# Kernel tuning notes

Measured on AMD Instinct MI355X. Metric: run time of the kernel, lower is better.

Reference implementation:

```python
import jax, jax.numpy as jnp
import numpy as np

BANDS = 103
FEATURE_DIM = 20
NSPIX = 256
N_ITER = 5
EPS = 1e-8


def _conv(x, w):
    # NCHW conv, SAME padding, stride 1
    return jax.lax.conv_general_dilated(x, w, (1, 1), 'SAME',
                                         dimension_numbers=('NCHW', 'OIHW', 'NCHW'))


def _aconv_bn_relu(x, k7, k5, k3, b, g, beta):
    # AConv: parallel 7x7 + 5x5 + 3x3 convs summed, then BatchNorm (batch stats) + ReLU
    y = _conv(x, k7) + _conv(x, k5) + _conv(x, k3) + b[None, :, None, None]
    mu = y.mean(axis=(0, 2, 3), keepdims=True)
    var = y.var(axis=(0, 2, 3), keepdims=True)
    y = (y - mu) * jax.lax.rsqrt(var + 1e-5) * g[None, :, None, None] + beta[None, :, None, None]
    return jax.nn.relu(y)


def _lsg_iter(pf, nspix, n_iter):
    # SSN-style iterative superpixel clustering.
    # pf: [B, C, H, W] pixel features. Returns soft assignment Q: [B, nspix, H*W].
    B, C, H, W = pf.shape
    hs = ws = int(np.sqrt(nspix))
    # init centroids by block-averaging onto an hs x ws grid
    c0 = pf.reshape(B, C, hs, H // hs, ws, W // ws).mean(axis=(3, 5)).reshape(B, C, nspix)
    pix = pf.reshape(B, C, H * W)            # [B, C, N]
    pn2 = jnp.sum(pix * pix, axis=1)         # [B, N]

    def dist(c):
        cn2 = jnp.sum(c * c, axis=1)                      # [B, S]
        dot = jnp.einsum('bcn,bcs->bsn', pix, c)          # [B, S, N]
        return pn2[:, None, :] - 2.0 * dot + cn2[:, :, None]

    def body(c, _):
        Q = jax.nn.softmax(-dist(c), axis=1)              # soft pixel->superpixel assignment
        cn = jnp.einsum('bsn,bcn->bcs', Q, pix) / (jnp.sum(Q, axis=2)[:, None, :] + EPS)
        return cn, None

    c, _ = jax.lax.scan(body, c0, None, length=n_iter)
    return jax.nn.softmax(-dist(c), axis=1)


def setup_inputs() -> dict:
    key = jax.random.key(0)
    ks = jax.random.split(key, 24)
    inp = {'x': jax.random.normal(ks[0], (1, BANDS, 256, 256), jnp.float32)}
    i = 1
    for name, ic, oc in (('s1', BANDS, 32), ('s2', 32, 32), ('s3', 64, 32)):
        for ksz in (7, 5, 3):
            inp[f'{name}_k{ksz}'] = jax.random.normal(ks[i], (oc, ic, ksz, ksz), jnp.float32) * 0.05
            i += 1
        inp[f'{name}_b'] = jnp.zeros((oc,), jnp.float32)
        inp[f'{name}_g'] = jnp.ones((oc,), jnp.float32)
        inp[f'{name}_beta'] = jnp.zeros((oc,), jnp.float32)
    inp['out_w'] = jax.random.normal(ks[i], (FEATURE_DIM - 5, 96, 1, 1), jnp.float32) * 0.05
    inp['out_b'] = jnp.zeros((FEATURE_DIM - 5,), jnp.float32)
    return inp


def reference(x, s1_k7, s1_k5, s1_k3, s1_b, s1_g, s1_beta,
              s2_k7, s2_k5, s2_k3, s2_b, s2_g, s2_beta,
              s3_k7, s3_k5, s3_k3, s3_b, s3_g, s3_beta,
              out_w, out_b):
    s1 = _aconv_bn_relu(x, s1_k7, s1_k5, s1_k3, s1_b, s1_g, s1_beta)
    s2 = _aconv_bn_relu(s1, s2_k7, s2_k5, s2_k3, s2_b, s2_g, s2_beta)
    s3 = _aconv_bn_relu(jnp.concatenate([s1, s2], axis=1), s3_k7, s3_k5, s3_k3, s3_b, s3_g, s3_beta)
    s4 = jnp.concatenate([s1, s2, s3], axis=1)                         # [B, 96, H, W]
    feat = jax.nn.relu(_conv(s4, out_w) + out_b[None, :, None, None])  # [B, feature_dim-5, H, W]
    pf = jnp.concatenate([feat, x], axis=1)                            # [B, feature_dim-5+bands, H, W]
    return _lsg_iter(pf, NSPIX, N_ITER)
```

## Files before the change

kernel.cpp:

```cpp
#include <hip/hip_runtime.h>

#define HW 65536

typedef short bf16x8 __attribute__((ext_vector_type(8)));
typedef float f32x4 __attribute__((ext_vector_type(4)));
typedef unsigned short u16x8 __attribute__((ext_vector_type(8)));

__device__ inline unsigned short f2bf(float v) {
    unsigned u = __float_as_uint(v);
    unsigned r = (u + 0x7FFF + ((u >> 16) & 1)) >> 16;
    return (unsigned short)r;
}
__device__ inline float ubf(unsigned short h) {
    return __uint_as_float(((unsigned)h) << 16);
}
__device__ inline uint4 pack8(const unsigned short* p) {
    uint4 u;
    u.x = (unsigned)p[0] | ((unsigned)p[1] << 16);
    u.y = (unsigned)p[2] | ((unsigned)p[3] << 16);
    u.z = (unsigned)p[4] | ((unsigned)p[5] << 16);
    u.w = (unsigned)p[6] | ((unsigned)p[7] << 16);
    return u;
}
__device__ inline size_t pfchoff(int c, int n) {
    return ((size_t)(n >> 5) << 12) + (c << 5) + (n & 31);
}

__global__ void wmerge_kernel(const float* __restrict__ k7, const float* __restrict__ k5,
                              const float* __restrict__ k3, int Cin, int nch,
                              unsigned short* __restrict__ wTh, unsigned short* __restrict__ wTl)
{
    int idx = blockIdx.x * 256 + threadIdx.x;
    int total = 49 * nch * 1024;
    if (idx >= total) return;
    int e = idx & 7;
    int lane = (idx >> 3) & 63;
    int octile = (idx >> 9) & 1;
    int chunk = (idx >> 10) % nch;
    int tap = idx / (nch << 10);
    int oc = octile * 16 + (lane & 15);
    int ci = chunk * 32 + (lane >> 4) * 8 + e;
    int ky = tap / 7, kx = tap % 7;
    float v = 0.f;
    if (ci < Cin) {
        v = k7[(oc * Cin + ci) * 49 + tap];
        if (ky >= 1 && ky <= 5 && kx >= 1 && kx <= 5)
            v += k5[(oc * Cin + ci) * 25 + (ky - 1) * 5 + (kx - 1)];
        if (ky >= 2 && ky <= 4 && kx >= 2 && kx <= 4)
            v += k3[(oc * Cin + ci) * 9 + (ky - 2) * 3 + (kx - 2)];
    }
    unsigned short h = f2bf(v);
    wTh[idx] = h;
    wTl[idx] = f2bf(v - ubf(h));
}

__global__ __launch_bounds__(256) void transpose_kernel(
    const float* __restrict__ x,
    unsigned short* __restrict__ xTh, unsigned short* __restrict__ xTl,
    unsigned short* __restrict__ pfch)
{
    __shared__ float buf[64 * 105];
    int t = threadIdx.x;
    int px0 = blockIdx.x * 64;
    for (int i = t; i < 103 * 64; i += 256) {
        int c = i >> 6, lane = i & 63;
        int n = px0 + lane;
        float v = x[(size_t)c * HW + n];
        buf[lane * 105 + c] = v;
        pfch[pfchoff(c, n)] = f2bf(v);
    }
    __syncthreads();
    int px = t >> 2, seg = t & 3;
    unsigned short h[32], l[32];
#pragma unroll
    for (int j = 0; j < 32; ++j) {
        int c = seg * 32 + j;
        float v = (c < 103) ? buf[px * 105 + c] : 0.f;
        h[j] = f2bf(v);
        l[j] = f2bf(v - ubf(h[j]));
    }
    size_t base = (size_t)(px0 + px) * 128 + seg * 32;
#pragma unroll
    for (int k = 0; k < 4; ++k) {
        *(uint4*)(xTh + base + k * 8) = pack8(h + k * 8);
        *(uint4*)(xTl + base + k * 8) = pack8(l + k * 8);
    }
}

__global__ __launch_bounds__(256) void convm_kernel(
    const unsigned short* __restrict__ actH, const unsigned short* __restrict__ actL,
    int Cs,
    const unsigned short* __restrict__ wTh, const unsigned short* __restrict__ wTl,
    int nchw,
    int c0a, int c1a, int t0a, int t1a,
    int c0b, int c1b, int t0b, int t1b,
    float* __restrict__ ypart)
{
    __shared__ __align__(16) unsigned short sH[22 * 704];
    __shared__ __align__(16) unsigned short sL[22 * 704];
    __shared__ __align__(16) unsigned short sW[3 * 2048];
    int t = threadIdx.x;
    int w = t >> 6, l = t & 63;
    int lc = l & 15, lg = l >> 4;
    int bid = blockIdx.x;
    int swz = (bid & 7) * 32 + (bid >> 3);
    int bx = swz & 15, byy = swz >> 4;
    int x0 = bx * 16, y0 = byy * 16;
    int z = blockIdx.y;
    int ch0 = z ? c0b : c0a, ch1 = z ? c1b : c1a;
    int tap0 = z ? t0b : t0a, tap1 = z ? t1b : t1a;
    float* yp = ypart + (size_t)z * 32 * HW;

    f32x4 a_hh[2][4], a_lh[2][4], a_hl[2][4];
#pragma unroll
    for (int ot = 0; ot < 2; ++ot)
#pragma unroll
        for (int rr = 0; rr < 4; ++rr)
#pragma unroll
            for (int r = 0; r < 4; ++r) {
                a_hh[ot][rr][r] = 0.f; a_lh[ot][rr][r] = 0.f; a_hl[ot][rr][r] = 0.f;
            }

    for (int ch = ch0; ch < ch1; ++ch) {
        int ci0 = ch * 32;
        __syncthreads();
        for (int i = t; i < 2 * 22 * 88; i += 256) {
            int pl = (i >= 22 * 88) ? 1 : 0;
            int j = pl ? i - 22 * 88 : i;
            int row = j / 88;
            int rem = j - row * 88;
            int px = rem >> 2, q = rem & 3;
            int gy = y0 - 3 + row, gx = x0 - 3 + px;
            uint4 v = {0u, 0u, 0u, 0u};
            if (gy >= 0 && gy < 256 && gx >= 0 && gx < 256) {
                const unsigned short* src = pl ? actL : actH;
                v = *(const uint4*)(src + (size_t)(gy * 256 + gx) * Cs + ci0 + q * 8);
            }
            unsigned short* dst = pl ? sL : sH;
            *(uint4*)(dst + row * 704 + q * 176 + px * 8) = v;
        }

        for (int g = tap0; g < tap1; g += 3) {
            int ge = g + 3; if (ge > tap1) ge = tap1;
            if (g > tap0) __syncthreads();
            for (int i = t; i < (ge - g) * 256; i += 256) {
                int tp = i >> 8, r = i & 255;
                const unsigned short* src = (r < 128) ? wTh : wTl;
                *(uint4*)(sW + tp * 2048 + r * 8) =
                    *(const uint4*)(src + ((size_t)((g + tp) * nchw + ch)) * 1024 + (r & 127) * 8);
            }
            __syncthreads();

            for (int tap = g; tap < ge; ++tap) {
                const unsigned short* wb = sW + (tap - g) * 2048 + l * 8;
                bf16x8 ah0 = *(const bf16x8*)(wb);
                bf16x8 ah1 = *(const bf16x8*)(wb + 512);
                bf16x8 al0 = *(const bf16x8*)(wb + 1024);
                bf16x8 al1 = *(const bf16x8*)(wb + 1536);
                int ky = tap / 7;
                int kx = tap - ky * 7;
#pragma unroll
                for (int rr = 0; rr < 4; ++rr) {
                    int off = (w * 4 + rr + ky) * 704 + lg * 176 + (lc + kx) * 8;
                    bf16x8 xh = *(const bf16x8*)(sH + off);
                    bf16x8 xl = *(const bf16x8*)(sL + off);
                    a_hh[0][rr] = __builtin_amdgcn_mfma_f32_16x16x32_bf16(ah0, xh, a_hh[0][rr], 0, 0, 0);
                    a_hh[1][rr] = __builtin_amdgcn_mfma_f32_16x16x32_bf16(ah1, xh, a_hh[1][rr], 0, 0, 0);
                    a_lh[0][rr] = __builtin_amdgcn_mfma_f32_16x16x32_bf16(al0, xh, a_lh[0][rr], 0, 0, 0);
                    a_lh[1][rr] = __builtin_amdgcn_mfma_f32_16x16x32_bf16(al1, xh, a_lh[1][rr], 0, 0, 0);
                    a_hl[0][rr] = __builtin_amdgcn_mfma_f32_16x16x32_bf16(ah0, xl, a_hl[0][rr], 0, 0, 0);
                    a_hl[1][rr] = __builtin_amdgcn_mfma_f32_16x16x32_bf16(ah1, xl, a_hl[1][rr], 0, 0, 0);
                }
            }
        }
    }

#pragma unroll
    for (int ot = 0; ot < 2; ++ot)
#pragma unroll
        for (int rr = 0; rr < 4; ++rr) {
            int n = (y0 + w * 4 + rr) * 256 + x0 + lc;
#pragma unroll
            for (int r = 0; r < 4; ++r) {
                int oc = ot * 16 + lg * 4 + r;
                yp[(size_t)oc * HW + n] = a_hh[ot][rr][r] + a_lh[ot][rr][r] + a_hl[ot][rr][r];
            }
        }
}

__global__ __launch_bounds__(256) void reduce2_kernel(
    const float* __restrict__ p0, const float* __restrict__ p1,
    float* __restrict__ y, float* __restrict__ ssum, float* __restrict__ ssq)
{
    int c = blockIdx.x >> 5, seg = blockIdx.x & 31;
    int base = c * HW + seg * 2048 + threadIdx.x * 8;
    float s = 0.f, q = 0.f;
#pragma unroll
    for (int h = 0; h < 2; ++h) {
        int o = base + h * 4;
        float4 a0 = *(const float4*)&p0[o];
        float4 a1 = *(const float4*)&p1[o];
        float4 v;
        v.x = a0.x + a1.x; v.y = a0.y + a1.y;
        v.z = a0.z + a1.z; v.w = a0.w + a1.w;
        *(float4*)&y[o] = v;
        s += v.x + v.y + v.z + v.w;
        q = fmaf(v.x, v.x, q); q = fmaf(v.y, v.y, q);
        q = fmaf(v.z, v.z, q); q = fmaf(v.w, v.w, q);
    }
#pragma unroll
    for (int d = 32; d >= 1; d >>= 1) {
        s += __shfl_down(s, d);
        q += __shfl_down(q, d);
    }
    __shared__ float ls[4], lq[4];
    int w = threadIdx.x >> 6;
    if ((threadIdx.x & 63) == 0) { ls[w] = s; lq[w] = q; }
    __syncthreads();
    if (threadIdx.x == 0) {
        atomicAdd(&ssum[c], ls[0] + ls[1] + ls[2] + ls[3]);
        atomicAdd(&ssq[c], lq[0] + lq[1] + lq[2] + lq[3]);
    }
}

__global__ void bnp_kernel(const float* __restrict__ ssum, const float* __restrict__ ssq,
                           const float* __restrict__ g, const float* __restrict__ beta,
                           float* __restrict__ scl, float* __restrict__ shf)
{
    int c = threadIdx.x;
    float mu  = ssum[c] * (1.f / 65536.f);
    float var = ssq[c] * (1.f / 65536.f) - mu * mu;
    float s = g[c] * rsqrtf(var + 1e-5f);
    scl[c] = s;
    shf[c] = beta[c] - mu * s;
}

__global__ __launch_bounds__(256) void bna_kernel(
    const float* __restrict__ yraw, const float* __restrict__ scl, const float* __restrict__ shf,
    unsigned short* __restrict__ aH, unsigned short* __restrict__ aL, int Cs, int slot0)
{
    int t = threadIdx.x;
    int lane = t & 63, cg = t >> 6;
    int px = blockIdx.x * 64 + lane;
    unsigned short h[8], l[8];
#pragma unroll
    for (int j = 0; j < 8; ++j) {
        int c = cg * 8 + j;
        float v = fmaxf(yraw[(size_t)c * HW + px] * scl[c] + shf[c], 0.f);
        h[j] = f2bf(v);
        l[j] = f2bf(v - ubf(h[j]));
    }
    *(uint4*)(aH + (size_t)px * Cs + slot0 + cg * 8) = pack8(h);
    *(uint4*)(aL + (size_t)px * Cs + slot0 + cg * 8) = pack8(l);
}

__global__ __launch_bounds__(256) void feat_kernel(
    const unsigned short* __restrict__ a12H, const unsigned short* __restrict__ a12L,
    const unsigned short* __restrict__ a3H, const unsigned short* __restrict__ a3L,
    const float* __restrict__ w, const float* __restrict__ b,
    unsigned short* __restrict__ xTh, unsigned short* __restrict__ xTl,
    unsigned short* __restrict__ pfch)
{
    int n = blockIdx.x * 256 + threadIdx.x;
    float facc[15];
#pragma unroll
    for (int oc = 0; oc < 15; ++oc) facc[oc] = b[oc];

#pragma unroll
    for (int k = 0; k < 12; ++k) {
        uint4 uh, ul;
        if (k < 8) {
            uh = *(const uint4*)(a12H + (size_t)n * 64 + k * 8);
            ul = *(const uint4*)(a12L + (size_t)n * 64 + k * 8);
        } else {
            uh = *(const uint4*)(a3H + (size_t)n * 32 + (k - 8) * 8);
            ul = *(const uint4*)(a3L + (size_t)n * 32 + (k - 8) * 8);
        }
        unsigned hw_[4] = {uh.x, uh.y, uh.z, uh.w};
        unsigned lw_[4] = {ul.x, ul.y, ul.z, ul.w};
#pragma unroll
        for (int j = 0; j < 8; ++j) {
            unsigned short hh = (unsigned short)(hw_[j >> 1] >> ((j & 1) * 16));
            unsigned short ll = (unsigned short)(lw_[j >> 1] >> ((j & 1) * 16));
            float av = ubf(hh) + ubf(ll);
#pragma unroll
            for (int oc = 0; oc < 15; ++oc)
                facc[oc] = fmaf(av, w[oc * 96 + k * 8 + j], facc[oc]);
        }
    }
    unsigned short fh[16], fl[16];
#pragma unroll
    for (int oc = 0; oc < 15; ++oc) {
        float v = fmaxf(facc[oc], 0.f);
        fh[oc] = f2bf(v);
        fl[oc] = f2bf(v - ubf(fh[oc]));
    }
    fh[15] = 0; fl[15] = 0;

    size_t base = (size_t)n * 128;
    uint4 h0 = *(const uint4*)(xTh + base + 96);
    uint4 l0 = *(const uint4*)(xTl + base + 96);
    h0.w = (h0.w & 0xFFFFu) | ((unsigned)fh[0] << 16);
    l0.w = (l0.w & 0xFFFFu) | ((unsigned)fl[0] << 16);
    *(uint4*)(xTh + base + 96) = h0;
    *(uint4*)(xTl + base + 96) = l0;
    *(uint4*)(xTh + base + 104) = pack8(fh + 1);
    *(uint4*)(xTl + base + 104) = pack8(fl + 1);
    unsigned short t2h[8], t2l[8];
#pragma unroll
    for (int j = 0; j < 8; ++j) {
        t2h[j] = (j < 6) ? fh[9 + j] : (unsigned short)0;
        t2l[j] = (j < 6) ? fl[9 + j] : (unsigned short)0;
    }
    *(uint4*)(xTh + base + 112) = pack8(t2h);
    *(uint4*)(xTl + base + 112) = pack8(t2l);
    unsigned short t3h[8] = {0, 0, 0, 0, 0, 0, 0, 0x3F80};
    unsigned short t3l[8] = {0, 0, 0, 0, 0, 0, 0, 0};
    *(uint4*)(xTh + base + 120) = pack8(t3h);
    *(uint4*)(xTl + base + 120) = pack8(t3l);

#pragma unroll
    for (int k2 = 0; k2 < 15; ++k2)
        pfch[pfchoff(103 + k2, n)] = fh[k2];
    pfch[pfchoff(118, n)] = 0x3F80;
#pragma unroll
    for (int c = 119; c < 128; ++c)
        pfch[pfchoff(c, n)] = 0;
}

__global__ __launch_bounds__(256) void c0_kernel(
    const unsigned short* __restrict__ pfTh, const unsigned short* __restrict__ pfTl,
    float* __restrict__ cn_fin)
{
    int s = blockIdx.x;
    int sy = s >> 4, sx = s & 15;
    int t = threadIdx.x;
    int xx = t >> 4;
    int cs = (t & 15) * 8;

    float acc[8];
#pragma unroll
    for (int j = 0; j < 8; ++j) acc[j] = 0.f;

    for (int yy = 0; yy < 16; ++yy) {
        int n = (sy * 16 + yy) * 256 + sx * 16 + xx;
        u16x8 h = *(const u16x8*)(pfTh + (size_t)n * 128 + cs);
        u16x8 l = *(const u16x8*)(pfTl + (size_t)n * 128 + cs);
#pragma unroll
        for (int j = 0; j < 8; ++j)
            acc[j] += ubf(h[j]) + ubf(l[j]);
    }
#pragma unroll
    for (int j = 0; j < 8; ++j) {
        acc[j] += __shfl_xor(acc[j], 16);
        acc[j] += __shfl_xor(acc[j], 32);
    }
    __shared__ float red[4][128];
    int w = t >> 6;
    if ((t & 63) < 16) {
#pragma unroll
        for (int j = 0; j < 8; ++j)
            red[w][(t & 15) * 8 + j] = acc[j];
    }
    __syncthreads();
    if (t < 128)
        cn_fin[s * 128 + t] = red[0][t] + red[1][t] + red[2][t] + red[3][t];
}

__global__ __launch_bounds__(128) void prep_kernel(
    const float* __restrict__ src,
    unsigned short* __restrict__ chiT, unsigned short* __restrict__ cloT,
    float scale0)
{
    int s = blockIdx.x, c = threadIdx.x;
    float v = src[s * 128 + c];
    v = (c < 118) ? v * scale0 : 0.f;
    float a = v * v;
#pragma unroll
    for (int d = 1; d < 64; d <<= 1) a += __shfl_xor(a, d);
    __shared__ float red[2];
    if ((c & 63) == 0) red[c >> 6] = a;
    __syncthreads();
    float tot = red[0] + red[1];
    unsigned short h, lo;
    if (c == 127) {
        float m2 = -0.5f * tot;
        h = f2bf(m2);
        lo = f2bf(m2 - ubf(h));
    } else {
        h = f2bf(v);
        lo = f2bf(v - ubf(h));
    }
    chiT[s * 128 + c] = h;
    cloT[s * 128 + c] = lo;
}

__global__ __launch_bounds__(128) void redprep_kernel(
    const float* __restrict__ cn_part,
    unsigned short* __restrict__ chiT, unsigned short* __restrict__ cloT)
{
    int s = blockIdx.x, c = threadIdx.x;
    float a = 0.f;
    for (int k = 0; k < 256; ++k)
        a += cn_part[(size_t)k * 32768 + s * 128 + c];
    __shared__ float sums[128];
    sums[c] = a;
    __syncthreads();
    float inv = 1.f / (sums[118] + 1e-8f);
    float v = (c < 118) ? a * inv : 0.f;
    float q = v * v;
#pragma unroll
    for (int d = 1; d < 64; d <<= 1) q += __shfl_xor(q, d);
    __shared__ float red[2];
    if ((c & 63) == 0) red[c >> 6] = q;
    __syncthreads();
    float tot = red[0] + red[1];
    unsigned short h, lo;
    if (c == 127) {
        float m2 = -0.5f * tot;
        h = f2bf(m2);
        lo = f2bf(m2 - ubf(h));
    } else {
        h = f2bf(v);
        lo = f2bf(v - ubf(h));
    }
    chiT[s * 128 + c] = h;
    cloT[s * 128 + c] = lo;
}

__global__ __launch_bounds__(512) void distcn_kernel(
    const unsigned short* __restrict__ chiT, const unsigned short* __restrict__ cloT,
    const unsigned short* __restrict__ pfTh, const unsigned short* __restrict__ pfTl,
    const unsigned short* __restrict__ pfch,
    float* __restrict__ cn_part, float* __restrict__ qf, int final_mode)
{
    __shared__ __align__(16) unsigned short sA[16384];
    unsigned short* sQ = sA;
    int t = threadIdx.x;
    int w = t >> 6, l = t & 63;
    int lc = l & 15, lg = l >> 4;
    int nblk = blockIdx.x * 256;
    int n0 = nblk + w * 32;

    bf16x8 bh[4][2], bl[4][2];
#pragma unroll
    for (int ks = 0; ks < 4; ++ks) {
        int kb = ks * 32 + 8 * lg;
        bh[ks][0] = *(const bf16x8*)(pfTh + (size_t)(n0 + lc) * 128 + kb);
        bh[ks][1] = *(const bf16x8*)(pfTh + (size_t)(n0 + 16 + lc) * 128 + kb);
        bl[ks][0] = *(const bf16x8*)(pfTl + (size_t)(n0 + lc) * 128 + kb);
        bl[ks][1] = *(const bf16x8*)(pfTl + (size_t)(n0 + 16 + lc) * 128 + kb);
    }

    f32x4 acc[16][2];
#pragma unroll
    for (int i = 0; i < 16; ++i)
#pragma unroll
        for (int g = 0; g < 2; ++g)
#pragma unroll
            for (int j = 0; j < 4; ++j) acc[i][g][j] = 0.f;

#pragma unroll
    for (int ro = 0; ro < 4; ++ro) {
        __syncthreads();
        for (int i = t; i < 2048; i += 512) {
            int plane = i >> 10;
            int ii = i & 1023;
            int sl = ii >> 4;
            int j = ii & 15;
            const unsigned short* src = plane ? cloT : chiT;
            uint4 v = *(const uint4*)(src + (((size_t)(ro * 64 + sl)) << 7) + j * 8);
            int ds = ((sl << 7) + j * 8) ^ ((sl & 7) << 3);
            *(uint4*)(sA + plane * 8192 + ds) = v;
        }
        __syncthreads();

#pragma unroll
        for (int s4 = 0; s4 < 4; ++s4) {
            const int st = ro * 4 + s4;
#pragma unroll
            for (int ks = 0; ks < 4; ++ks) {
                int e0 = (((s4 * 16 + lc) << 7) + ks * 32 + lg * 8) ^ ((lc & 7) << 3);
                bf16x8 ah = *(const bf16x8*)(sA + e0);
                bf16x8 al = *(const bf16x8*)(sA + 8192 + e0);
                acc[st][0] = __builtin_amdgcn_mfma_f32_16x16x32_bf16(ah, bh[ks][0], acc[st][0], 0, 0, 0);
                acc[st][0] = __builtin_amdgcn_mfma_f32_16x16x32_bf16(al, bh[ks][0], acc[st][0], 0, 0, 0);
                acc[st][0] = __builtin_amdgcn_mfma_f32_16x16x32_bf16(ah, bl[ks][0], acc[st][0], 0, 0, 0);
                acc[st][1] = __builtin_amdgcn_mfma_f32_16x16x32_bf16(ah, bh[ks][1], acc[st][1], 0, 0, 0);
                acc[st][1] = __builtin_amdgcn_mfma_f32_16x16x32_bf16(al, bh[ks][1], acc[st][1], 0, 0, 0);
                acc[st][1] = __builtin_amdgcn_mfma_f32_16x16x32_bf16(ah, bl[ks][1], acc[st][1], 0, 0, 0);
            }
        }
    }

    float m0 = -1e30f, m1 = -1e30f;
#pragma unroll
    for (int st = 0; st < 16; ++st)
#pragma unroll
        for (int r = 0; r < 4; ++r) {
            m0 = fmaxf(m0, acc[st][0][r]);
            m1 = fmaxf(m1, acc[st][1][r]);
        }
    m0 = fmaxf(m0, __shfl_xor(m0, 16)); m0 = fmaxf(m0, __shfl_xor(m0, 32));
    m1 = fmaxf(m1, __shfl_xor(m1, 16)); m1 = fmaxf(m1, __shfl_xor(m1, 32));

    float s0 = 0.f, s1 = 0.f;
#pragma unroll
    for (int st = 0; st < 16; ++st)
#pragma unroll
        for (int r = 0; r < 4; ++r) {
            float e0 = __expf(2.f * (acc[st][0][r] - m0));
            float e1 = __expf(2.f * (acc[st][1][r] - m1));
            acc[st][0][r] = e0; acc[st][1][r] = e1;
            s0 += e0; s1 += e1;
        }
    s0 += __shfl_xor(s0, 16); s0 += __shfl_xor(s0, 32);
    s1 += __shfl_xor(s1, 16); s1 += __shfl_xor(s1, 32);
    float i0 = 1.f / s0, i1 = 1.f / s1;

    if (final_mode) {
        int nA = n0 + lc, nB = n0 + 16 + lc;
#pragma unroll
        for (int st = 0; st < 16; ++st)
#pragma unroll
            for (int r = 0; r < 4; ++r) {
                int s = st * 16 + lg * 4 + r;
                qf[(size_t)s * HW + nA] = acc[st][0][r] * i0;
                qf[(size_t)s * HW + nB] = acc[st][1][r] * i1;
            }
        return;
    }

    bf16x8 pb[8];
#pragma unroll
    for (int kc = 0; kc < 8; ++kc)
        pb[kc] = *(const bf16x8*)(pfch + (((size_t)((nblk >> 5) + kc)) << 12)
                                  + (w * 16 + lc) * 32 + lg * 8);

#pragma unroll
    for (int h = 0; h < 4; ++h) {
        __syncthreads();
#pragma unroll
        for (int s4 = 0; s4 < 4; ++s4) {
            const int st = h * 4 + s4;
#pragma unroll
            for (int g = 0; g < 2; ++g) {
                float iv = g ? i1 : i0;
#pragma unroll
                for (int r = 0; r < 4; ++r) {
                    int idx = ((s4 * 8 + w) * 64 + (g * 2 + (lc >> 3)) * 16 + lg * 4 + r) * 8 + (lc & 7);
                    sQ[idx] = f2bf(acc[st][g][r] * iv);
                }
            }
        }
        __syncthreads();

        f32x4 a2[4];
#pragma unroll
        for (int i = 0; i < 4; ++i)
#pragma unroll
            for (int j = 0; j < 4; ++j) a2[i][j] = 0.f;

#pragma unroll
        for (int kc = 0; kc < 8; ++kc) {
#pragma unroll
            for (int s4 = 0; s4 < 4; ++s4) {
                bf16x8 afr = *(const bf16x8*)(sQ + ((size_t)(s4 * 8 + kc) * 64 + l) * 8);
                a2[s4] = __builtin_amdgcn_mfma_f32_16x16x32_bf16(afr, pb[kc], a2[s4], 0, 0, 0);
            }
        }

        float* out = cn_part + (size_t)blockIdx.x * 32768;
#pragma unroll
        for (int s4 = 0; s4 < 4; ++s4)
#pragma unroll
            for (int r = 0; r < 4; ++r) {
                int s = (h * 4 + s4) * 16 + lg * 4 + r;
                int c = w * 16 + lc;
                out[s * 128 + c] = a2[s4][r];
            }
    }
}

extern "C" void kernel_launch(void* const* d_in, const int* in_sizes, int n_in,
                              void* d_out, int out_size, void* d_ws, size_t ws_size,
                              hipStream_t stream)
{
    const float* x     = (const float*)d_in[0];
    const float* s1k7  = (const float*)d_in[1];
    const float* s1k5  = (const float*)d_in[2];
    const float* s1k3  = (const float*)d_in[3];
    const float* s1g   = (const float*)d_in[5];
    const float* s1be  = (const float*)d_in[6];
    const float* s2k7  = (const float*)d_in[7];
    const float* s2k5  = (const float*)d_in[8];
    const float* s2k3  = (const float*)d_in[9];
    const float* s2g   = (const float*)d_in[11];
    const float* s2be  = (const float*)d_in[12];
    const float* s3k7  = (const float*)d_in[13];
    const float* s3k5  = (const float*)d_in[14];
    const float* s3k3  = (const float*)d_in[15];
    const float* s3g   = (const float*)d_in[17];
    const float* s3be  = (const float*)d_in[18];
    const float* outw  = (const float*)d_in[19];
    const float* outb  = (const float*)d_in[20];

    float* ws = (float*)d_ws;
    size_t off = 0;
    unsigned short* wT1h = (unsigned short*)(ws + off); off += 100352;
    unsigned short* wT1l = (unsigned short*)(ws + off); off += 100352;
    unsigned short* wT2h = (unsigned short*)(ws + off); off += 25088;
    unsigned short* wT2l = (unsigned short*)(ws + off); off += 25088;
    unsigned short* wT3h = (unsigned short*)(ws + off); off += 50176;
    unsigned short* wT3l = (unsigned short*)(ws + off); off += 50176;
    float* stats = ws + off; off += 192;
    float* bn    = ws + off; off += 192;
    float* cn_fin= ws + off; off += 32768;
    unsigned short* chiT = (unsigned short*)(ws + off); off += 16384;
    unsigned short* cloT = (unsigned short*)(ws + off); off += 16384;
    unsigned short* xTh  = (unsigned short*)(ws + off); off += 4194304;
    unsigned short* xTl  = (unsigned short*)(ws + off); off += 4194304;
    unsigned short* pfch = (unsigned short*)(ws + off); off += 4194304;
    unsigned short* a12H = (unsigned short*)(ws + off); off += 2097152;
    unsigned short* a12L = (unsigned short*)(ws + off); off += 2097152;

    char* ob = (char*)d_out;
    float* p0   = (float*)ob;
    float* p1   = (float*)(ob + (size_t)8 * 1024 * 1024);
    float* ysum = (float*)(ob + (size_t)16 * 1024 * 1024);
    float* cn_part = (float*)ob;
    float* qf = (float*)ob;
    unsigned short* a3H = (unsigned short*)(ob + (size_t)32 * 1024 * 1024);
    unsigned short* a3L = a3H + (size_t)HW * 32;

    hipMemsetAsync(stats, 0, 192 * sizeof(float), stream);
    wmerge_kernel<<<(49 * 4 * 1024 + 255) / 256, 256, 0, stream>>>(s1k7, s1k5, s1k3, 103, 4, wT1h, wT1l);
    wmerge_kernel<<<(49 * 1 * 1024 + 255) / 256, 256, 0, stream>>>(s2k7, s2k5, s2k3, 32, 1, wT2h, wT2l);
    wmerge_kernel<<<(49 * 2 * 1024 + 255) / 256, 256, 0, stream>>>(s3k7, s3k5, s3k3, 64, 2, wT3h, wT3l);

    transpose_kernel<<<1024, 256, 0, stream>>>(x, xTh, xTl, pfch);

    convm_kernel<<<dim3(256, 2), 256, 0, stream>>>(xTh, xTl, 128, wT1h, wT1l, 4,
                                                   0, 2, 0, 49, 2, 4, 0, 49, p0);
    reduce2_kernel<<<1024, 256, 0, stream>>>(p0, p1, ysum, stats + 0, stats + 32);
    bnp_kernel<<<1, 32, 0, stream>>>(stats + 0, stats + 32, s1g, s1be, bn + 0, bn + 32);
    bna_kernel<<<1024, 256, 0, stream>>>(ysum, bn + 0, bn + 32, a12H, a12L, 64, 0);

    convm_kernel<<<dim3(256, 2), 256, 0, stream>>>(a12H, a12L, 64, wT2h, wT2l, 1,
                                                   0, 1, 0, 25, 0, 1, 25, 49, p0);
    reduce2_kernel<<<1024, 256, 0, stream>>>(p0, p1, ysum, stats + 64, stats + 96);
    bnp_kernel<<<1, 32, 0, stream>>>(stats + 64, stats + 96, s2g, s2be, bn + 64, bn + 96);
    bna_kernel<<<1024, 256, 0, stream>>>(ysum, bn + 64, bn + 96, a12H, a12L, 64, 32);

    convm_kernel<<<dim3(256, 2), 256, 0, stream>>>(a12H, a12L, 64, wT3h, wT3l, 2,
                                                   0, 1, 0, 49, 1, 2, 0, 49, p0);
    reduce2_kernel<<<1024, 256, 0, stream>>>(p0, p1, ysum, stats + 128, stats + 160);
    bnp_kernel<<<1, 32, 0, stream>>>(stats + 128, stats + 160, s3g, s3be, bn + 128, bn + 160);
    bna_kernel<<<1024, 256, 0, stream>>>(ysum, bn + 128, bn + 160, a3H, a3L, 32, 0);

    feat_kernel<<<256, 256, 0, stream>>>(a12H, a12L, a3H, a3L, outw, outb, xTh, xTl, pfch);
    c0_kernel<<<256, 256, 0, stream>>>(xTh, xTl, cn_fin);
    prep_kernel<<<256, 128, 0, stream>>>(cn_fin, chiT, cloT, 1.f / 256.f);

    for (int it = 0; it < 5; ++it) {
        distcn_kernel<<<256, 512, 0, stream>>>(chiT, cloT, xTh, xTl, pfch, cn_part, qf, 0);
        redprep_kernel<<<256, 128, 0, stream>>>(cn_part, chiT, cloT);
    }
    distcn_kernel<<<256, 512, 0, stream>>>(chiT, cloT, xTh, xTl, pfch, cn_part, qf, 1);
}
```

Before: 512.8 us.

## Double-buffer LDS centroid tiles and Q staging in distcn kernel

Splits the shared-memory buffer into two halves and software-pipelines both phases of the distance/centroid kernel. The next centroid tile is prefetched from global memory into registers while MFMAs run on the current tile, and the next Q slab is written to LDS while the current one is consumed. This removes one barrier per stage and hides global load latency. The cost is double the LDS use (64KB per block), which may lower occupancy, plus extra staging registers.

After: 501.7 us. 2.2% less time.

```diff
diff --git a/kernel.cpp b/kernel.cpp
--- a/kernel.cpp
+++ b/kernel.cpp
@@ -434,8 +434,8 @@
     const unsigned short* __restrict__ pfch,
     float* __restrict__ cn_part, float* __restrict__ qf, int final_mode)
 {
-    __shared__ __align__(16) unsigned short sA[16384];
-    unsigned short* sQ = sA;
+    __shared__ __align__(16) unsigned short sA0[16384];
+    __shared__ __align__(16) unsigned short sA1[16384];
     int t = threadIdx.x;
     int w = t >> 6, l = t & 63;
     int lc = l & 15, lg = l >> 4;
@@ -452,6 +452,18 @@
         bl[ks][1] = *(const bf16x8*)(pfTl + (size_t)(n0 + 16 + lc) * 128 + kb);
     }
 
+    int sti[4], std_[4];
+#pragma unroll
+    for (int k = 0; k < 4; ++k) {
+        int i = t + k * 512;
+        int plane = i >> 10;
+        int ii = i & 1023;
+        int sl = ii >> 4;
+        int j = ii & 15;
+        sti[k] = (plane << 16) | (sl << 4) | j;
+        std_[k] = plane * 8192 + (((sl << 7) + j * 8) ^ ((sl & 7) << 3));
+    }
+
     f32x4 acc[16][2];
 #pragma unroll
     for (int i = 0; i < 16; ++i)
@@ -460,20 +472,36 @@
 #pragma unroll
             for (int j = 0; j < 4; ++j) acc[i][g][j] = 0.f;
 
+    {
+#pragma unroll
+        for (int k = 0; k < 4; ++k) {
+            int plane = sti[k] >> 16;
+            int sl = (sti[k] >> 4) & 0xFFF;
+            int j = sti[k] & 15;
+            const unsigned short* src = plane ? cloT : chiT;
+            uint4 v = *(const uint4*)(src + (((size_t)sl) << 7) + j * 8);
+            unsigned short* dst = sA0;
+            *(uint4*)(dst + std_[k]) = v;
+        }
+    }
+    __syncthreads();
+
 #pragma unroll
     for (int ro = 0; ro < 4; ++ro) {
-        __syncthreads();
-        for (int i = t; i < 2048; i += 512) {
-            int plane = i >> 10;
-            int ii = i & 1023;
-            int sl = ii >> 4;
-            int j = ii & 15;
-            const unsigned short* src = plane ? cloT : chiT;
-            uint4 v = *(const uint4*)(src + (((size_t)(ro * 64 + sl)) << 7) + j * 8);
-            int ds = ((sl << 7) + j * 8) ^ ((sl & 7) << 3);
-            *(uint4*)(sA + plane * 8192 + ds) = v;
-        }
-        __syncthreads();
+        unsigned short* cur = (ro & 1) ? sA1 : sA0;
+        unsigned short* nxt = (ro & 1) ? sA0 : sA1;
+
+        uint4 stg[4];
+        if (ro < 3) {
+#pragma unroll
+            for (int k = 0; k < 4; ++k) {
+                int plane = sti[k] >> 16;
+                int sl = (sti[k] >> 4) & 0xFFF;
+                int j = sti[k] & 15;
+                const unsigned short* src = plane ? cloT : chiT;
+                stg[k] = *(const uint4*)(src + (((size_t)((ro + 1) * 64 + sl)) << 7) + j * 8);
+            }
+        }
 
 #pragma unroll
         for (int s4 = 0; s4 < 4; ++s4) {
@@ -481,8 +509,8 @@
 #pragma unroll
             for (int ks = 0; ks < 4; ++ks) {
                 int e0 = (((s4 * 16 + lc) << 7) + ks * 32 + lg * 8) ^ ((lc & 7) << 3);
-                bf16x8 ah = *(const bf16x8*)(sA + e0);
-                bf16x8 al = *(const bf16x8*)(sA + 8192 + e0);
+                bf16x8 ah = *(const bf16x8*)(cur + e0);
+                bf16x8 al = *(const bf16x8*)(cur + 8192 + e0);
                 acc[st][0] = __builtin_amdgcn_mfma_f32_16x16x32_bf16(ah, bh[ks][0], acc[st][0], 0, 0, 0);
                 acc[st][0] = __builtin_amdgcn_mfma_f32_16x16x32_bf16(al, bh[ks][0], acc[st][0], 0, 0, 0);
                 acc[st][0] = __builtin_amdgcn_mfma_f32_16x16x32_bf16(ah, bl[ks][0], acc[st][0], 0, 0, 0);
@@ -491,6 +519,13 @@
                 acc[st][1] = __builtin_amdgcn_mfma_f32_16x16x32_bf16(ah, bl[ks][1], acc[st][1], 0, 0, 0);
             }
         }
+
+        if (ro < 3) {
+#pragma unroll
+            for (int k = 0; k < 4; ++k)
+                *(uint4*)(nxt + std_[k]) = stg[k];
+        }
+        __syncthreads();
     }
 
     float m0 = -1e30f, m1 = -1e30f;
@@ -538,22 +573,39 @@
                                   + (w * 16 + lc) * 32 + lg * 8);
 
 #pragma unroll
+    for (int s4 = 0; s4 < 4; ++s4) {
+#pragma unroll
+        for (int g = 0; g < 2; ++g) {
+            float iv = g ? i1 : i0;
+#pragma unroll
+            for (int r = 0; r < 4; ++r) {
+                int idx = ((s4 * 8 + w) * 64 + (g * 2 + (lc >> 3)) * 16 + lg * 4 + r) * 8 + (lc & 7);
+                sA0[idx] = f2bf(acc[s4][g][r] * iv);
+            }
+        }
+    }
+    __syncthreads();
+
+#pragma unroll
     for (int h = 0; h < 4; ++h) {
-        __syncthreads();
-#pragma unroll
-        for (int s4 = 0; s4 < 4; ++s4) {
-            const int st = h * 4 + s4;
-#pragma unroll
-            for (int g = 0; g < 2; ++g) {
-                float iv = g ? i1 : i0;
-#pragma unroll
-                for (int r = 0; r < 4; ++r) {
-                    int idx = ((s4 * 8 + w) * 64 + (g * 2 + (lc >> 3)) * 16 + lg * 4 + r) * 8 + (lc & 7);
-                    sQ[idx] = f2bf(acc[st][g][r] * iv);
+        unsigned short* curQ = (h & 1) ? sA1 : sA0;
+        unsigned short* nxtQ = (h & 1) ? sA0 : sA1;
+
+        if (h < 3) {
+#pragma unroll
+            for (int s4 = 0; s4 < 4; ++s4) {
+                const int st = (h + 1) * 4 + s4;
+#pragma unroll
+                for (int g = 0; g < 2; ++g) {
+                    float iv = g ? i1 : i0;
+#pragma unroll
+                    for (int r = 0; r < 4; ++r) {
+                        int idx = ((s4 * 8 + w) * 64 + (g * 2 + (lc >> 3)) * 16 + lg * 4 + r) * 8 + (lc & 7);
+                        nxtQ[idx] = f2bf(acc[st][g][r] * iv);
+                    }
                 }
             }
         }
-        __syncthreads();
 
         f32x4 a2[4];
 #pragma unroll
@@ -565,7 +617,7 @@
         for (int kc = 0; kc < 8; ++kc) {
 #pragma unroll
             for (int s4 = 0; s4 < 4; ++s4) {
-                bf16x8 afr = *(const bf16x8*)(sQ + ((size_t)(s4 * 8 + kc) * 64 + l) * 8);
+                bf16x8 afr = *(const bf16x8*)(curQ + ((size_t)(s4 * 8 + kc) * 64 + l) * 8);
                 a2[s4] = __builtin_amdgcn_mfma_f32_16x16x32_bf16(afr, pb[kc], a2[s4], 0, 0, 0);
             }
         }
@@ -579,6 +631,7 @@
                 int c = w * 16 + lc;
                 out[s * 128 + c] = a2[s4][r];
             }
+        __syncthreads();
     }
 }
 
```
